# Kernel optimization log

Hardware: AMD Instinct MI355X
Metric: run time of the kernel (lower is better)

The kernel has to match this reference:

```python
import jax, jax.numpy as jnp
import numpy as np

B, S, E, H, F = 8, 1024, 1024, 16, 4096
D = E // H  # head_dim = 64
EPS = 1e-5


def setup_inputs() -> dict:
    key = jax.random.key(0)
    ks = jax.random.split(key, 12)
    s = 0.02
    return {
        "x": jax.random.normal(ks[0], (B, S, E), dtype=jnp.float32),
        # per-head projections (shared across heads), torch stores [out,in]; we use [in,out]
        "Wq": jax.random.normal(ks[1], (D, D), dtype=jnp.float32) * s,
        "Wk": jax.random.normal(ks[2], (D, D), dtype=jnp.float32) * s,
        "Wv": jax.random.normal(ks[3], (D, D), dtype=jnp.float32) * s,
        "Wo": jax.random.normal(ks[4], (E, E), dtype=jnp.float32) * s,
        "bo": jnp.zeros((E,), dtype=jnp.float32),
        "W1": jax.random.normal(ks[5], (E, F), dtype=jnp.float32) * s,
        "b1": jnp.zeros((F,), dtype=jnp.float32),
        "W2": jax.random.normal(ks[6], (F, E), dtype=jnp.float32) * s,
        "b2": jnp.zeros((E,), dtype=jnp.float32),
        "g1": jnp.ones((E,), dtype=jnp.float32),
        "beta1": jnp.zeros((E,), dtype=jnp.float32),
        "g2": jnp.ones((E,), dtype=jnp.float32),
        "beta2": jnp.zeros((E,), dtype=jnp.float32),
    }


def _layer_norm(x, g, b):
    m = jnp.mean(x, axis=-1, keepdims=True)
    v = jnp.mean(jnp.square(x - m), axis=-1, keepdims=True)
    return (x - m) * jax.lax.rsqrt(v + EPS) * g + b


def reference(x, Wq, Wk, Wv, Wo, bo, W1, b1, W2, b2, g1, beta1, g2, beta2):
    b, s, e = x.shape
    # --- attention sublayer (pre-norm) ---
    nx = _layer_norm(x, g1, beta1)
    h = nx.reshape(b, s, H, D)              # [B,S,H,D]
    q = h @ Wq                               # per-head linear, weight shared over heads
    k = h @ Wk
    v = h @ Wv
    energy = jnp.einsum('bqhd,bkhd->bhqk', q, k)  # full [B,H,S,S] scores
    mask = jnp.tril(jnp.ones((s, s), dtype=bool))
    energy = jnp.where(mask, energy, -jnp.inf)
    att = jax.nn.softmax(energy / jnp.sqrt(jnp.float32(e)), axis=-1)  # NOTE: scale by sqrt(embed_dim)
    o = jnp.einsum('bhqk,bkhd->bqhd', att, v).reshape(b, s, e)
    x = x + (o @ Wo + bo)
    # --- MLP sublayer (pre-norm); dropout is identity in eval ---
    nx = _layer_norm(x, g2, beta2)
    x = x + (jax.nn.relu(nx @ W1 + b1) @ W2 + b2)
    return x
```

## Files before the change

kernel.cpp:

```cpp
#include <hip/hip_runtime.h>

typedef unsigned short u16;
typedef __attribute__((ext_vector_type(4))) float f4;
typedef __attribute__((ext_vector_type(8))) short s8v;
typedef __attribute__((ext_vector_type(4))) unsigned short u16x4;

#define DEVINL __device__ __forceinline__

DEVINL float b2f(u16 u) { union { unsigned i; float f; } x; x.i = ((unsigned)u) << 16; return x.f; }
DEVINL u16 f2b(float f) {
  union { float f; unsigned i; } x; x.f = f;
  unsigned r = 0x7FFFu + ((x.i >> 16) & 1u);
  return (u16)((x.i + r) >> 16);
}

#define GLD_LDS16(g, l)                                                        \
  __builtin_amdgcn_global_load_lds((__attribute__((address_space(1))) void*)(g), \
                                   (__attribute__((address_space(3))) void*)(l), 16, 0, 0)

__global__ __launch_bounds__(256) void k_transpose(const float* __restrict__ in,
                                                   u16* __restrict__ out, int R, int C) {
  __shared__ float t[32][33];
  int tx = threadIdx.x & 31, ty = threadIdx.x >> 5;
  int c0 = blockIdx.x * 32, r0 = blockIdx.y * 32;
#pragma unroll
  for (int i = 0; i < 32; i += 8)
    t[ty + i][tx] = in[(long)(r0 + ty + i) * C + (c0 + tx)];
  __syncthreads();
#pragma unroll
  for (int i = 0; i < 32; i += 8)
    out[(long)(c0 + ty + i) * R + (r0 + tx)] = f2b(t[tx][ty + i]);
}

__global__ __launch_bounds__(256) void k_vtrans(const u16* __restrict__ v, u16* __restrict__ vt) {
  __shared__ u16 t[64][72];
  int bh = blockIdx.x, b = bh >> 4, h = bh & 15;
  int s0 = blockIdx.y * 64;
  int tid = threadIdx.x;
#pragma unroll
  for (int p = 0; p < 2; ++p) {
    int idx = p * 256 + tid;
    int sl = idx >> 3, c8 = (idx & 7) * 8;
    *(s8v*)(&t[sl][c8]) = *(const s8v*)(v + (((long)(b * 1024 + s0 + sl) * 16 + h) * 64) + c8);
  }
  __syncthreads();
#pragma unroll
  for (int p = 0; p < 2; ++p) {
    int idx = p * 256 + tid;
    int d = idx >> 3, c8 = (idx & 7) * 8;
    s8v o;
#pragma unroll
    for (int e = 0; e < 8; ++e) o[e] = (short)t[c8 + e][d];
    *(s8v*)(vt + ((long)bh * 64 + d) * 1024 + s0 + c8) = o;
  }
}

__global__ __launch_bounds__(256) void k_layernorm(const float* __restrict__ x,
                                                   const float* __restrict__ g,
                                                   const float* __restrict__ be,
                                                   u16* __restrict__ out) {
  long row = blockIdx.x;
  int tid = threadIdx.x;
  f4 v = ((const f4*)(x + row * 1024))[tid];
  float s = v[0] + v[1] + v[2] + v[3];
  float s2 = v[0] * v[0] + v[1] * v[1] + v[2] * v[2] + v[3] * v[3];
#pragma unroll
  for (int off = 32; off > 0; off >>= 1) {
    s += __shfl_down(s, off, 64);
    s2 += __shfl_down(s2, off, 64);
  }
  __shared__ float red[8];
  int wv = tid >> 6, ln = tid & 63;
  if (ln == 0) { red[wv] = s; red[4 + wv] = s2; }
  __syncthreads();
  s = red[0] + red[1] + red[2] + red[3];
  s2 = red[4] + red[5] + red[6] + red[7];
  float mean = s * (1.0f / 1024.0f);
  float var = s2 * (1.0f / 1024.0f) - mean * mean;
  float rs = rsqrtf(var + 1e-5f);
  f4 gg = ((const f4*)g)[tid];
  f4 bb = ((const f4*)be)[tid];
  u16x4 o;
#pragma unroll
  for (int i = 0; i < 4; ++i) o[i] = f2b((v[i] - mean) * rs * gg[i] + bb[i]);
  ((u16x4*)(out + row * 1024))[tid] = o;
}

__global__ __launch_bounds__(256) void k_qkv(const u16* __restrict__ nx, const u16* __restrict__ WqT,
                                             const u16* __restrict__ WkT, const u16* __restrict__ WvT,
                                             u16* __restrict__ q, u16* __restrict__ k,
                                             u16* __restrict__ v) {
  int tid = threadIdx.x, lane = tid & 63, wave = tid >> 6;
  int quad = lane >> 4, l16 = lane & 15;
  long rbase = (long)blockIdx.x * 64 + wave * 16;
  s8v a0 = *(const s8v*)(nx + (rbase + l16) * 64 + quad * 8);
  s8v a1 = *(const s8v*)(nx + (rbase + l16) * 64 + 32 + quad * 8);
  const u16* Ws[3] = {WqT, WkT, WvT};
  u16* Os[3] = {q, k, v};
#pragma unroll
  for (int t = 0; t < 3; ++t) {
#pragma unroll
    for (int j = 0; j < 4; ++j) {
      s8v b0 = *(const s8v*)(Ws[t] + (j * 16 + l16) * 64 + quad * 8);
      s8v b1 = *(const s8v*)(Ws[t] + (j * 16 + l16) * 64 + 32 + quad * 8);
      f4 acc = {0.f, 0.f, 0.f, 0.f};
      acc = __builtin_amdgcn_mfma_f32_16x16x32_bf16(a0, b0, acc, 0, 0, 0);
      acc = __builtin_amdgcn_mfma_f32_16x16x32_bf16(a1, b1, acc, 0, 0, 0);
#pragma unroll
      for (int r = 0; r < 4; ++r)
        Os[t][(rbase + quad * 4 + r) * 64 + j * 16 + l16] = f2b(acc[r]);
    }
  }
}

__global__ __launch_bounds__(256) void k_attn_mfma(const u16* __restrict__ q,
                                                   const u16* __restrict__ kk,
                                                   const u16* __restrict__ vt,
                                                   u16* __restrict__ o) {
  constexpr int LDK = 72;
  __shared__ u16 Ks[64 * LDK];
  __shared__ u16 Vt[64 * LDK];
  __shared__ u16 Ps[4][16 * LDK];
  int tid = threadIdx.x, lane = tid & 63, wave = tid >> 6;
  int quad = lane >> 4, l16 = lane & 15;
  int b = blockIdx.x >> 4, h = blockIdx.x & 15;
  int qi = (int)gridDim.y - 1 - (int)blockIdx.y;
  int q0 = qi * 64 + wave * 16;

  const u16* qp = q + (((long)(b * 1024 + q0 + l16)) * 16 + h) * 64;
  s8v aq0 = *(const s8v*)(qp + quad * 8);
  s8v aq1 = *(const s8v*)(qp + 32 + quad * 8);

  f4 O[4];
  float m_[4], l_[4];
#pragma unroll
  for (int jd = 0; jd < 4; ++jd) O[jd] = f4{0.f, 0.f, 0.f, 0.f};
#pragma unroll
  for (int r = 0; r < 4; ++r) { m_[r] = -__builtin_inff(); l_[r] = 0.f; }

  for (int kt = 0; kt <= qi; ++kt) {
    __syncthreads();
#pragma unroll
    for (int p = 0; p < 2; ++p) {
      int idx = p * 256 + tid;
      int row = idx >> 3, c8 = (idx & 7) * 8;
      *(s8v*)(Ks + row * LDK + c8) =
          *(const s8v*)(kk + (((long)(b * 1024 + kt * 64 + row)) * 16 + h) * 64 + c8);
      *(s8v*)(Vt + row * LDK + c8) =
          *(const s8v*)(vt + ((long)blockIdx.x * 64 + row) * 1024 + kt * 64 + c8);
    }
    __syncthreads();

    f4 sf[4];
#pragma unroll
    for (int jn = 0; jn < 4; ++jn) {
      s8v b0 = *(const s8v*)(Ks + (jn * 16 + l16) * LDK + quad * 8);
      s8v b1 = *(const s8v*)(Ks + (jn * 16 + l16) * LDK + 32 + quad * 8);
      f4 acc = f4{0.f, 0.f, 0.f, 0.f};
      acc = __builtin_amdgcn_mfma_f32_16x16x32_bf16(aq0, b0, acc, 0, 0, 0);
      acc = __builtin_amdgcn_mfma_f32_16x16x32_bf16(aq1, b1, acc, 0, 0, 0);
      sf[jn] = acc;
    }
    bool diag = (kt == qi);
    float rm[4];
#pragma unroll
    for (int r = 0; r < 4; ++r) rm[r] = -__builtin_inff();
#pragma unroll
    for (int jn = 0; jn < 4; ++jn)
#pragma unroll
      for (int r = 0; r < 4; ++r) {
        float v = sf[jn][r] * 0.03125f;
        if (diag && (jn * 16 + l16 > wave * 16 + quad * 4 + r)) v = -__builtin_inff();
        sf[jn][r] = v;
        rm[r] = fmaxf(rm[r], v);
      }
#pragma unroll
    for (int off = 1; off < 16; off <<= 1)
#pragma unroll
      for (int r = 0; r < 4; ++r) rm[r] = fmaxf(rm[r], __shfl_xor(rm[r], off, 64));
    float alpha[4], rs[4];
#pragma unroll
    for (int r = 0; r < 4; ++r) {
      float mn = fmaxf(m_[r], rm[r]);
      alpha[r] = __expf(m_[r] - mn);
      m_[r] = mn;
      rs[r] = 0.f;
    }
#pragma unroll
    for (int jn = 0; jn < 4; ++jn)
#pragma unroll
      for (int r = 0; r < 4; ++r) {
        float p = __expf(sf[jn][r] - m_[r]);
        rs[r] += p;
        Ps[wave][(quad * 4 + r) * LDK + jn * 16 + l16] = f2b(p);
      }
#pragma unroll
    for (int off = 1; off < 16; off <<= 1)
#pragma unroll
      for (int r = 0; r < 4; ++r) rs[r] += __shfl_xor(rs[r], off, 64);
#pragma unroll
    for (int r = 0; r < 4; ++r) l_[r] = l_[r] * alpha[r] + rs[r];
#pragma unroll
    for (int jd = 0; jd < 4; ++jd)
#pragma unroll
      for (int r = 0; r < 4; ++r) O[jd][r] *= alpha[r];
    asm volatile("s_waitcnt lgkmcnt(0)" ::: "memory");
    s8v p0 = *(const s8v*)(&Ps[wave][l16 * LDK + quad * 8]);
    s8v p1 = *(const s8v*)(&Ps[wave][l16 * LDK + 32 + quad * 8]);
#pragma unroll
    for (int jd = 0; jd < 4; ++jd) {
      s8v b0 = *(const s8v*)(Vt + (jd * 16 + l16) * LDK + quad * 8);
      s8v b1 = *(const s8v*)(Vt + (jd * 16 + l16) * LDK + 32 + quad * 8);
      O[jd] = __builtin_amdgcn_mfma_f32_16x16x32_bf16(p0, b0, O[jd], 0, 0, 0);
      O[jd] = __builtin_amdgcn_mfma_f32_16x16x32_bf16(p1, b1, O[jd], 0, 0, 0);
    }
  }
#pragma unroll
  for (int r = 0; r < 4; ++r) {
    float inv = 1.0f / l_[r];
    u16* op = o + (((long)(b * 1024 + q0 + quad * 4 + r)) * 16 + h) * 64;
#pragma unroll
    for (int jd = 0; jd < 4; ++jd) op[jd * 16 + l16] = f2b(O[jd][r] * inv);
  }
}

template <int EPI>
__global__ __launch_bounds__(256) void k_gemm_bt(const u16* __restrict__ A, const u16* __restrict__ BT,
                                                 const float* __restrict__ bias,
                                                 const float* __restrict__ resid,
                                                 void* __restrict__ outp, int M, int N, int K) {
  __shared__ u16 sA[3][128 * 32];
  __shared__ u16 sB[3][128 * 32];
  int tid = threadIdx.x, lane = tid & 63, wave = tid >> 6;
  int quad = lane >> 4, l16 = lane & 15;
  int wm = wave >> 1, wn = wave & 1;
  long bm = blockIdx.x, bn = blockIdx.y;
  int srow = tid >> 2, scol = (tid & 3) * 8;
  const u16* ga = A + (bm * 128 + srow) * (long)K + scol;
  const u16* gb = BT + (bn * 128 + srow) * (long)K + scol;
  int woff = wave * 1024;

  f4 acc[4][4];
#pragma unroll
  for (int i = 0; i < 4; ++i)
#pragma unroll
    for (int j = 0; j < 4; ++j) acc[i][j] = f4{0.f, 0.f, 0.f, 0.f};

#pragma unroll
  for (int t = 0; t < 2; ++t) {
    char* lA = (char*)&sA[t][0] + woff;
    char* lB = (char*)&sB[t][0] + woff;
    GLD_LDS16(ga + t * 32, lA);
    GLD_LDS16(ga + 64 * (long)K + t * 32, lA + 4096);
    GLD_LDS16(gb + t * 32, lB);
    GLD_LDS16(gb + 64 * (long)K + t * 32, lB + 4096);
  }

  int cur = 0;
  for (int k0 = 0; k0 < K; k0 += 32) {
    int k2 = k0 + 64;
    if (k2 < K) {
      asm volatile("s_waitcnt vmcnt(4)\n\ts_barrier" ::: "memory");
      int nb = cur >= 1 ? cur - 1 : 2;
      char* lA = (char*)&sA[nb][0] + woff;
      char* lB = (char*)&sB[nb][0] + woff;
      GLD_LDS16(ga + k2, lA);
      GLD_LDS16(ga + 64 * (long)K + k2, lA + 4096);
      GLD_LDS16(gb + k2, lB);
      GLD_LDS16(gb + 64 * (long)K + k2, lB + 4096);
    } else {
      asm volatile("s_waitcnt vmcnt(0)\n\ts_barrier" ::: "memory");
    }
    const u16* cA = sA[cur];
    const u16* cB = sB[cur];
    s8v aF[4], bF[4];
#pragma unroll
    for (int i = 0; i < 4; ++i)
      aF[i] = *(const s8v*)(cA + (wm * 64 + i * 16 + l16) * 32 + quad * 8);
#pragma unroll
    for (int j = 0; j < 4; ++j)
      bF[j] = *(const s8v*)(cB + (wn * 64 + j * 16 + l16) * 32 + quad * 8);
#pragma unroll
    for (int i = 0; i < 4; ++i)
#pragma unroll
      for (int j = 0; j < 4; ++j)
        acc[i][j] = __builtin_amdgcn_mfma_f32_16x16x32_bf16(aF[i], bF[j], acc[i][j], 0, 0, 0);
    cur = cur < 2 ? cur + 1 : 0;
  }

#pragma unroll
  for (int i = 0; i < 4; ++i) {
#pragma unroll
    for (int j = 0; j < 4; ++j) {
      long row = bm * 128 + wm * 64 + i * 16 + quad * 4;
      int col = (int)bn * 128 + wn * 64 + j * 16 + l16;
      float bcol = bias[col];
#pragma unroll
      for (int r = 0; r < 4; ++r) {
        float val = acc[i][j][r] + bcol;
        if (EPI == 1) {
          ((u16*)outp)[(row + r) * (long)N + col] = f2b(val > 0.f ? val : 0.f);
        } else {
          ((float*)outp)[(row + r) * (long)N + col] = resid[(row + r) * (long)N + col] + val;
        }
      }
    }
  }
}

extern "C" void kernel_launch(void* const* d_in, const int* in_sizes, int n_in, void* d_out,
                              int out_size, void* d_ws, size_t ws_size, hipStream_t stream) {
  const float* x = (const float*)d_in[0];
  const float* Wq = (const float*)d_in[1];
  const float* Wk = (const float*)d_in[2];
  const float* Wv = (const float*)d_in[3];
  const float* Wo = (const float*)d_in[4];
  const float* bo = (const float*)d_in[5];
  const float* W1 = (const float*)d_in[6];
  const float* b1 = (const float*)d_in[7];
  const float* W2 = (const float*)d_in[8];
  const float* b2 = (const float*)d_in[9];
  const float* g1 = (const float*)d_in[10];
  const float* be1 = (const float*)d_in[11];
  const float* g2 = (const float*)d_in[12];
  const float* be2 = (const float*)d_in[13];

  char* ws = (char*)d_ws;
  const size_t MB = 1ull << 20;
  u16* nx = (u16*)(ws + 0);
  u16* qb = (u16*)(ws + 16 * MB);
  u16* kb = (u16*)(ws + 32 * MB);
  u16* vb = (u16*)(ws + 48 * MB);
  float* x1 = (float*)(ws + 64 * MB);
  u16* h1 = (u16*)(ws + 96 * MB);
  u16* vtr = (u16*)(ws + 96 * MB);
  u16* WoT = (u16*)(ws + 160 * MB);
  u16* W1T = (u16*)(ws + 162 * MB);
  u16* W2T = (u16*)(ws + 170 * MB);
  u16* WqT = (u16*)(ws + 178 * MB);
  u16* WkT = WqT + 64 * 64;
  u16* WvT = WkT + 64 * 64;
  u16* ob = nx;
  u16* nx2 = qb;

  k_transpose<<<dim3(32, 32), 256, 0, stream>>>(Wo, WoT, 1024, 1024);
  k_transpose<<<dim3(128, 32), 256, 0, stream>>>(W1, W1T, 1024, 4096);
  k_transpose<<<dim3(32, 128), 256, 0, stream>>>(W2, W2T, 4096, 1024);
  k_transpose<<<dim3(2, 2), 256, 0, stream>>>(Wq, WqT, 64, 64);
  k_transpose<<<dim3(2, 2), 256, 0, stream>>>(Wk, WkT, 64, 64);
  k_transpose<<<dim3(2, 2), 256, 0, stream>>>(Wv, WvT, 64, 64);

  k_layernorm<<<8192, 256, 0, stream>>>(x, g1, be1, nx);
  k_qkv<<<2048, 256, 0, stream>>>(nx, WqT, WkT, WvT, qb, kb, vb);
  k_vtrans<<<dim3(128, 16), 256, 0, stream>>>(vb, vtr);
  k_attn_mfma<<<dim3(128, 16), 256, 0, stream>>>(qb, kb, vtr, ob);
  k_gemm_bt<2><<<dim3(64, 8), 256, 0, stream>>>(ob, WoT, bo, x, x1, 8192, 1024, 1024);

  k_layernorm<<<8192, 256, 0, stream>>>(x1, g2, be2, nx2);
  k_gemm_bt<1><<<dim3(64, 32), 256, 0, stream>>>(nx2, W1T, b1, nullptr, h1, 8192, 4096, 1024);
  k_gemm_bt<2><<<dim3(64, 8), 256, 0, stream>>>(h1, W2T, b2, x1, d_out, 8192, 1024, 4096);
}
```

Measured before the change: 457.0 us.

## Load GEMM B fragments directly into registers and store residual x1 as bf16

The GEMM kernel stops staging the B (weight) tile through LDS. Each wave now loads its MFMA B fragments straight from global memory into a three-deep register pipeline, while A keeps its LDS triple buffer. This removes half the LDS traffic and LDS footprint, at the cost of more registers and non-coalesced 16-byte global loads that rely on cache reuse across blocks. Separately, the intermediate residual x1 is stored in bf16 instead of fp32 to cut its write and read traffic, which lowers residual precision.

After: 579.2 us. 1.27x slower.

```diff
diff --git a/kernel.cpp b/kernel.cpp
--- a/kernel.cpp
+++ b/kernel.cpp
@@ -55,13 +55,20 @@
   }
 }
 
-__global__ __launch_bounds__(256) void k_layernorm(const float* __restrict__ x,
+template <int IT>
+__global__ __launch_bounds__(256) void k_layernorm(const void* __restrict__ xv,
                                                    const float* __restrict__ g,
                                                    const float* __restrict__ be,
                                                    u16* __restrict__ out) {
   long row = blockIdx.x;
   int tid = threadIdx.x;
-  f4 v = ((const f4*)(x + row * 1024))[tid];
+  f4 v;
+  if (IT == 0) {
+    v = ((const f4*)((const float*)xv + row * 1024))[tid];
+  } else {
+    u16x4 t = ((const u16x4*)((const u16*)xv + row * 1024))[tid];
+    v = f4{b2f(t[0]), b2f(t[1]), b2f(t[2]), b2f(t[3])};
+  }
   float s = v[0] + v[1] + v[2] + v[3];
   float s2 = v[0] * v[0] + v[1] * v[1] + v[2] * v[2] + v[3] * v[3];
 #pragma unroll
@@ -227,17 +234,16 @@
 template <int EPI>
 __global__ __launch_bounds__(256) void k_gemm_bt(const u16* __restrict__ A, const u16* __restrict__ BT,
                                                  const float* __restrict__ bias,
-                                                 const float* __restrict__ resid,
+                                                 const void* __restrict__ residv,
                                                  void* __restrict__ outp, int M, int N, int K) {
   __shared__ u16 sA[3][128 * 32];
-  __shared__ u16 sB[3][128 * 32];
   int tid = threadIdx.x, lane = tid & 63, wave = tid >> 6;
   int quad = lane >> 4, l16 = lane & 15;
   int wm = wave >> 1, wn = wave & 1;
   long bm = blockIdx.x, bn = blockIdx.y;
   int srow = tid >> 2, scol = (tid & 3) * 8;
   const u16* ga = A + (bm * 128 + srow) * (long)K + scol;
-  const u16* gb = BT + (bn * 128 + srow) * (long)K + scol;
+  const u16* gbf = BT + (bn * 128 + wn * 64 + l16) * (long)K + quad * 8;
   int woff = wave * 1024;
 
   f4 acc[4][4];
@@ -246,45 +252,50 @@
 #pragma unroll
     for (int j = 0; j < 4; ++j) acc[i][j] = f4{0.f, 0.f, 0.f, 0.f};
 
-#pragma unroll
-  for (int t = 0; t < 2; ++t) {
-    char* lA = (char*)&sA[t][0] + woff;
-    char* lB = (char*)&sB[t][0] + woff;
-    GLD_LDS16(ga + t * 32, lA);
-    GLD_LDS16(ga + 64 * (long)K + t * 32, lA + 4096);
-    GLD_LDS16(gb + t * 32, lB);
-    GLD_LDS16(gb + 64 * (long)K + t * 32, lB + 4096);
-  }
+  s8v bcur[4], bn1[4], bn2[4];
+  {
+    char* lA = (char*)&sA[0][0] + woff;
+    GLD_LDS16(ga, lA);
+    GLD_LDS16(ga + 64 * (long)K, lA + 4096);
+  }
+#pragma unroll
+  for (int j = 0; j < 4; ++j) bcur[j] = *(const s8v*)(gbf + (long)j * 16 * K);
+  {
+    char* lA = (char*)&sA[1][0] + woff;
+    GLD_LDS16(ga + 32, lA);
+    GLD_LDS16(ga + 64 * (long)K + 32, lA + 4096);
+  }
+#pragma unroll
+  for (int j = 0; j < 4; ++j) bn1[j] = *(const s8v*)(gbf + (long)j * 16 * K + 32);
 
   int cur = 0;
   for (int k0 = 0; k0 < K; k0 += 32) {
-    int k2 = k0 + 64;
-    if (k2 < K) {
-      asm volatile("s_waitcnt vmcnt(4)\n\ts_barrier" ::: "memory");
-      int nb = cur >= 1 ? cur - 1 : 2;
-      char* lA = (char*)&sA[nb][0] + woff;
-      char* lB = (char*)&sB[nb][0] + woff;
-      GLD_LDS16(ga + k2, lA);
-      GLD_LDS16(ga + 64 * (long)K + k2, lA + 4096);
-      GLD_LDS16(gb + k2, lB);
-      GLD_LDS16(gb + 64 * (long)K + k2, lB + 4096);
+    if (k0 + 32 < K) {
+      asm volatile("s_waitcnt vmcnt(6)\n\ts_barrier" ::: "memory");
+      int k2 = k0 + 64;
+      if (k2 < K) {
+        int nb = cur >= 1 ? cur - 1 : 2;
+        char* lA = (char*)&sA[nb][0] + woff;
+        GLD_LDS16(ga + k2, lA);
+        GLD_LDS16(ga + 64 * (long)K + k2, lA + 4096);
+#pragma unroll
+        for (int j = 0; j < 4; ++j) bn2[j] = *(const s8v*)(gbf + (long)j * 16 * K + k2);
+      }
     } else {
       asm volatile("s_waitcnt vmcnt(0)\n\ts_barrier" ::: "memory");
     }
     const u16* cA = sA[cur];
-    const u16* cB = sB[cur];
-    s8v aF[4], bF[4];
+    s8v aF[4];
 #pragma unroll
     for (int i = 0; i < 4; ++i)
       aF[i] = *(const s8v*)(cA + (wm * 64 + i * 16 + l16) * 32 + quad * 8);
 #pragma unroll
-    for (int j = 0; j < 4; ++j)
-      bF[j] = *(const s8v*)(cB + (wn * 64 + j * 16 + l16) * 32 + quad * 8);
-#pragma unroll
     for (int i = 0; i < 4; ++i)
 #pragma unroll
       for (int j = 0; j < 4; ++j)
-        acc[i][j] = __builtin_amdgcn_mfma_f32_16x16x32_bf16(aF[i], bF[j], acc[i][j], 0, 0, 0);
+        acc[i][j] = __builtin_amdgcn_mfma_f32_16x16x32_bf16(aF[i], bcur[j], acc[i][j], 0, 0, 0);
+#pragma unroll
+    for (int j = 0; j < 4; ++j) { bcur[j] = bn1[j]; bn1[j] = bn2[j]; }
     cur = cur < 2 ? cur + 1 : 0;
   }
 
@@ -298,10 +309,14 @@
 #pragma unroll
       for (int r = 0; r < 4; ++r) {
         float val = acc[i][j][r] + bcol;
+        long idx = (row + r) * (long)N + col;
         if (EPI == 1) {
-          ((u16*)outp)[(row + r) * (long)N + col] = f2b(val > 0.f ? val : 0.f);
+          ((u16*)outp)[idx] = f2b(val > 0.f ? val : 0.f);
         } else {
-          ((float*)outp)[(row + r) * (long)N + col] = resid[(row + r) * (long)N + col] + val;
+          float rv = (EPI == 4) ? b2f(((const u16*)residv)[idx]) : ((const float*)residv)[idx];
+          float o = rv + val;
+          if (EPI == 3) ((u16*)outp)[idx] = f2b(o);
+          else ((float*)outp)[idx] = o;
         }
       }
     }
@@ -331,7 +346,7 @@
   u16* qb = (u16*)(ws + 16 * MB);
   u16* kb = (u16*)(ws + 32 * MB);
   u16* vb = (u16*)(ws + 48 * MB);
-  float* x1 = (float*)(ws + 64 * MB);
+  u16* x1b = (u16*)(ws + 64 * MB);
   u16* h1 = (u16*)(ws + 96 * MB);
   u16* vtr = (u16*)(ws + 96 * MB);
   u16* WoT = (u16*)(ws + 160 * MB);
@@ -350,13 +365,13 @@
   k_transpose<<<dim3(2, 2), 256, 0, stream>>>(Wk, WkT, 64, 64);
   k_transpose<<<dim3(2, 2), 256, 0, stream>>>(Wv, WvT, 64, 64);
 
-  k_layernorm<<<8192, 256, 0, stream>>>(x, g1, be1, nx);
+  k_layernorm<0><<<8192, 256, 0, stream>>>(x, g1, be1, nx);
   k_qkv<<<2048, 256, 0, stream>>>(nx, WqT, WkT, WvT, qb, kb, vb);
   k_vtrans<<<dim3(128, 16), 256, 0, stream>>>(vb, vtr);
   k_attn_mfma<<<dim3(128, 16), 256, 0, stream>>>(qb, kb, vtr, ob);
-  k_gemm_bt<2><<<dim3(64, 8), 256, 0, stream>>>(ob, WoT, bo, x, x1, 8192, 1024, 1024);
-
-  k_layernorm<<<8192, 256, 0, stream>>>(x1, g2, be2, nx2);
+  k_gemm_bt<3><<<dim3(64, 8), 256, 0, stream>>>(ob, WoT, bo, x, x1b, 8192, 1024, 1024);
+
+  k_layernorm<1><<<8192, 256, 0, stream>>>(x1b, g2, be2, nx2);
   k_gemm_bt<1><<<dim3(64, 32), 256, 0, stream>>>(nx2, W1T, b1, nullptr, h1, 8192, 4096, 1024);
-  k_gemm_bt<2><<<dim3(64, 8), 256, 0, stream>>>(h1, W2T, b2, x1, d_out, 8192, 1024, 4096);
-}
+  k_gemm_bt<4><<<dim3(64, 8), 256, 0, stream>>>(h1, W2T, b2, x1b, d_out, 8192, 1024, 4096);
+}
```
